# Kernel optimization log

Hardware: AMD Instinct MI355X
Metric: run time of the kernel (lower is better)

## Reference

```python
import jax, jax.numpy as jnp
import numpy as np

N_NODES = 50000
N_EDGES = 800000
IN_FEATS = 256
H_FEATS = 256
NUM_CLASSES = 128


def setup_inputs() -> dict:
    key = jax.random.key(0)
    ks = jax.random.split(key, 5)
    x = jax.random.normal(ks[0], (N_NODES, IN_FEATS), dtype=jnp.float32)
    src = jax.random.randint(ks[1], (N_EDGES,), 0, N_NODES, dtype=jnp.int64)
    dst = jax.random.randint(ks[2], (N_EDGES,), 0, N_NODES, dtype=jnp.int64)
    W1 = jax.random.normal(ks[3], (IN_FEATS, H_FEATS), dtype=jnp.float32) * (1.0 / np.sqrt(IN_FEATS))
    b1 = jnp.zeros((H_FEATS,), dtype=jnp.float32)
    W2 = jax.random.normal(ks[4], (H_FEATS, NUM_CLASSES), dtype=jnp.float32) * (1.0 / np.sqrt(H_FEATS))
    b2 = jnp.zeros((NUM_CLASSES,), dtype=jnp.float32)
    return {"x": x, "src": src, "dst": dst, "W1": W1, "b1": b1, "W2": W2, "b2": b2}


def _graph_conv(x, src, dst, norm_src, norm_dst, W, b):
    # DGL GraphConv, norm='both': D_out^{-1/2} A D_in^{-1/2} X W + b
    # project first (in_feats >= out_feats -> cheaper messages), math identical
    h = (x * norm_src[:, None]) @ W                      # [N, out]
    agg = jax.ops.segment_sum(h[src], dst, num_segments=N_NODES)  # gather + scatter-add
    return agg * norm_dst[:, None] + b


def reference(x, src, dst, W1, b1, W2, b2):
    ones = jnp.ones((N_EDGES,), dtype=x.dtype)
    deg_out = jax.ops.segment_sum(ones, src, num_segments=N_NODES)
    deg_in = jax.ops.segment_sum(ones, dst, num_segments=N_NODES)
    norm_src = jnp.clip(deg_out, 1.0, None) ** -0.5
    norm_dst = jnp.clip(deg_in, 1.0, None) ** -0.5

    h = _graph_conv(x, src, dst, norm_src, norm_dst, W1, b1)
    h = jax.nn.relu(h)
    out = _graph_conv(h, src, dst, norm_src, norm_dst, W2, b2)
    return out
```

## Files before the change

### kernel.cpp

```cpp
#include <hip/hip_runtime.h>

#define NNODES 50000
#define MPAD   50048
#define NEDGES 800000
#define KDIM   256
#define FH     256
#define FOUT   128

#define SHIFT  8
#define NBUCK  196
#define NB1    200
#define EPB    4000
#define CELLS  (NBUCK * NB1)
#define NSCAN  (2 * CELLS)
#define SCANB  ((NSCAN + 511) / 512)

typedef __bf16 bf16x8 __attribute__((ext_vector_type(8)));
typedef float floatx4 __attribute__((ext_vector_type(4)));

__device__ __forceinline__ float bf2f(unsigned short u) {
    union { unsigned int i; float f; } v;
    v.i = ((unsigned int)u) << 16;
    return v.f;
}
__device__ __forceinline__ unsigned short f2bf(float f) {
    union { float f; unsigned int i; } v;
    v.f = f;
    unsigned int r = v.i + 0x7FFFu + ((v.i >> 16) & 1u);
    return (unsigned short)(r >> 16);
}

__global__ __launch_bounds__(256) void l1_count(const int* __restrict__ src,
                                                const int* __restrict__ dst,
                                                int* __restrict__ cell) {
    __shared__ int histD[256], histS[256];
    const int b = blockIdx.x, tid = threadIdx.x;
    const int base = b * EPB;
    histD[tid] = 0; histS[tid] = 0;
    __syncthreads();
    for (int g = tid; g < EPB / 4; g += 256) {
        uint4 s4 = *(const uint4*)(src + base + g * 4);
        uint4 d4 = *(const uint4*)(dst + base + g * 4);
        atomicAdd(&histD[d4.x >> SHIFT], 1);
        atomicAdd(&histD[d4.y >> SHIFT], 1);
        atomicAdd(&histD[d4.z >> SHIFT], 1);
        atomicAdd(&histD[d4.w >> SHIFT], 1);
        atomicAdd(&histS[s4.x >> SHIFT], 1);
        atomicAdd(&histS[s4.y >> SHIFT], 1);
        atomicAdd(&histS[s4.z >> SHIFT], 1);
        atomicAdd(&histS[s4.w >> SHIFT], 1);
    }
    __syncthreads();
    if (tid < NBUCK) {
        cell[tid * NB1 + b] = histD[tid];
        cell[CELLS + tid * NB1 + b] = histS[tid];
    }
}

__global__ __launch_bounds__(512) void scanA(int* __restrict__ data,
                                             int* __restrict__ sums, int n) {
    __shared__ int s[512];
    int tid = threadIdx.x;
    int i = blockIdx.x * 512 + tid;
    int v = (i < n) ? data[i] : 0;
    s[tid] = v;
    __syncthreads();
    for (int off = 1; off < 512; off <<= 1) {
        int t = (tid >= off) ? s[tid - off] : 0;
        __syncthreads();
        s[tid] += t;
        __syncthreads();
    }
    if (i < n) data[i] = s[tid] - v;
    if (tid == 511) sums[blockIdx.x] = s[511];
}

__global__ __launch_bounds__(512) void scanB(int* __restrict__ sums, int nb) {
    __shared__ int s[512];
    int tid = threadIdx.x;
    int v = (tid < nb) ? sums[tid] : 0;
    s[tid] = v;
    __syncthreads();
    for (int off = 1; off < 512; off <<= 1) {
        int t = (tid >= off) ? s[tid - off] : 0;
        __syncthreads();
        s[tid] += t;
        __syncthreads();
    }
    if (tid < nb) sums[tid] = s[tid] - v;
}

__global__ __launch_bounds__(512) void scanC(int* __restrict__ data,
                                             const int* __restrict__ sums, int n) {
    int i = blockIdx.x * 512 + threadIdx.x;
    if (i < n) data[i] += sums[blockIdx.x];
}

__global__ __launch_bounds__(256) void l1_scatter(const int* __restrict__ src,
                                                  const int* __restrict__ dst,
                                                  const int* __restrict__ cell,
                                                  unsigned int* __restrict__ tmp1,
                                                  unsigned char* __restrict__ tmp2) {
    __shared__ int histD[256], histS[256];
    __shared__ int exD[256], exS[256];
    __shared__ unsigned int bufD[EPB];
    __shared__ unsigned short bufS[EPB];
    const int b = blockIdx.x, tid = threadIdx.x;
    const int base = b * EPB;

    histD[tid] = 0; histS[tid] = 0;
    __syncthreads();
    for (int g = tid; g < EPB / 4; g += 256) {
        uint4 s4 = *(const uint4*)(src + base + g * 4);
        uint4 d4 = *(const uint4*)(dst + base + g * 4);
        atomicAdd(&histD[d4.x >> SHIFT], 1);
        atomicAdd(&histD[d4.y >> SHIFT], 1);
        atomicAdd(&histD[d4.z >> SHIFT], 1);
        atomicAdd(&histD[d4.w >> SHIFT], 1);
        atomicAdd(&histS[s4.x >> SHIFT], 1);
        atomicAdd(&histS[s4.y >> SHIFT], 1);
        atomicAdd(&histS[s4.z >> SHIFT], 1);
        atomicAdd(&histS[s4.w >> SHIFT], 1);
    }
    __syncthreads();
    int vD = histD[tid], vS = histS[tid];
    exD[tid] = vD; exS[tid] = vS;
    __syncthreads();
    for (int off = 1; off < 256; off <<= 1) {
        int tD = (tid >= off) ? exD[tid - off] : 0;
        int tS = (tid >= off) ? exS[tid - off] : 0;
        __syncthreads();
        exD[tid] += tD; exS[tid] += tS;
        __syncthreads();
    }
    int eD = exD[tid] - vD, eS = exS[tid] - vS;
    __syncthreads();
    exD[tid] = eD; exS[tid] = eS;
    histD[tid] = eD; histS[tid] = eS;
    __syncthreads();
    for (int g = tid; g < EPB / 4; g += 256) {
        uint4 s4 = *(const uint4*)(src + base + g * 4);
        uint4 d4 = *(const uint4*)(dst + base + g * 4);
        unsigned int ss[4] = {s4.x, s4.y, s4.z, s4.w};
        unsigned int dd[4] = {d4.x, d4.y, d4.z, d4.w};
#pragma unroll
        for (int j = 0; j < 4; ++j) {
            int p = atomicAdd(&histD[dd[j] >> SHIFT], 1);
            bufD[p] = (ss[j] << 16) | dd[j];
            int q = atomicAdd(&histS[ss[j] >> SHIFT], 1);
            bufS[q] = (unsigned short)ss[j];
        }
    }
    __syncthreads();
    for (int e = tid; e < EPB; e += 256) {
        unsigned int p = bufD[e];
        int k = (p & 0xFFFFu) >> SHIFT;
        tmp1[cell[k * NB1 + b] + (e - exD[k])] = p;
    }
    for (int e = tid; e < EPB; e += 256) {
        unsigned int s = bufS[e];
        int k = s >> SHIFT;
        tmp2[(cell[CELLS + k * NB1 + b] - NEDGES) + (e - exS[k])] = (unsigned char)(s & 255u);
    }
}

__global__ __launch_bounds__(256) void l2_dst(const unsigned int* __restrict__ tmp1,
                                              const int* __restrict__ cell,
                                              int* __restrict__ row_ptr,
                                              float* __restrict__ norm_dst,
                                              int* __restrict__ csr_src) {
    __shared__ int cnt[256], ofs[256], cur[256];
    const int k = blockIdx.x, tid = threadIdx.x;
    const int start = cell[k * NB1];
    const int end = (k + 1 < NBUCK) ? cell[(k + 1) * NB1] : NEDGES;
    cnt[tid] = 0;
    __syncthreads();
    for (int e = start + tid; e < end; e += 256)
        atomicAdd(&cnt[tmp1[e] & 255u], 1);
    __syncthreads();
    int v = cnt[tid];
    ofs[tid] = v;
    __syncthreads();
    for (int off = 1; off < 256; off <<= 1) {
        int t = (tid >= off) ? ofs[tid - off] : 0;
        __syncthreads();
        ofs[tid] += t;
        __syncthreads();
    }
    int excl = ofs[tid] - v;
    int node = k * 256 + tid;
    if (node < NNODES) {
        row_ptr[node] = start + excl;
        int d = v < 1 ? 1 : v;
        norm_dst[node] = 1.0f / sqrtf((float)d);
    }
    cur[tid] = start + excl;
    if (k == 0 && tid == 0) row_ptr[NNODES] = NEDGES;
    __syncthreads();
    for (int e = start + tid; e < end; e += 256) {
        unsigned int p = tmp1[e];
        int pos = atomicAdd(&cur[p & 255u], 1);
        csr_src[pos] = (int)(p >> 16);
    }
}

__global__ __launch_bounds__(256) void l2_src(const unsigned char* __restrict__ tmp2,
                                              const int* __restrict__ cell,
                                              float* __restrict__ norm_src) {
    __shared__ int cnt[256];
    const int k = blockIdx.x, tid = threadIdx.x;
    const int start = cell[CELLS + k * NB1] - NEDGES;
    const int end = (k + 1 < NBUCK) ? cell[CELLS + (k + 1) * NB1] - NEDGES : NEDGES;
    cnt[tid] = 0;
    __syncthreads();
    for (int e = start + tid; e < end; e += 256)
        atomicAdd(&cnt[tmp2[e]], 1);
    __syncthreads();
    int node = k * 256 + tid;
    if (node < NNODES) {
        int d = cnt[tid] < 1 ? 1 : cnt[tid];
        norm_src[node] = 1.0f / sqrtf((float)d);
    }
}

__global__ __launch_bounds__(256) void cast_wt_both(const float* __restrict__ W1,
                                                    unsigned short* __restrict__ Wt1,
                                                    const float* __restrict__ W2,
                                                    unsigned short* __restrict__ Wt2) {
    __shared__ float tile[32][33];
    int b = blockIdx.x;
    const float* W; unsigned short* Wt; int N;
    if (b < 64) { W = W1; Wt = Wt1; N = FH; }
    else        { b -= 64; W = W2; Wt = Wt2; N = FOUT; }
    int kt = (b & 7) * 32;
    int nt = (b >> 3) * 32;
    int tx = threadIdx.x & 31;
    int ty = threadIdx.x >> 5;
    for (int r = ty; r < 32; r += 8)
        tile[r][tx] = W[(size_t)(kt + r) * N + nt + tx];
    __syncthreads();
    for (int r = ty; r < 32; r += 8)
        Wt[(size_t)(nt + r) * KDIM + kt + tx] = f2bf(tile[tx][r]);
}

__device__ __forceinline__ uint4 stage_a8(const float* A, int row, int k, float scale, bool valid) {
    if (!valid) return make_uint4(0u, 0u, 0u, 0u);
    const float* p = A + (size_t)row * KDIM + k;
    float4 v0 = *(const float4*)p;
    float4 v1 = *(const float4*)(p + 4);
    union { uint4 u; unsigned short s[8]; } r;
    r.s[0] = f2bf(v0.x * scale); r.s[1] = f2bf(v0.y * scale);
    r.s[2] = f2bf(v0.z * scale); r.s[3] = f2bf(v0.w * scale);
    r.s[4] = f2bf(v1.x * scale); r.s[5] = f2bf(v1.y * scale);
    r.s[6] = f2bf(v1.z * scale); r.s[7] = f2bf(v1.w * scale);
    return r.u;
}
__device__ __forceinline__ uint4 stage_a8(const unsigned short* A, int row, int k, float, bool) {
    return *(const uint4*)(A + (size_t)row * KDIM + k);
}

template <typename TA, bool SCALE>
__global__ __launch_bounds__(256) void gemm_mfma(const TA* __restrict__ A,
                                                 const unsigned short* __restrict__ Bt,
                                                 const float* __restrict__ norm,
                                                 unsigned short* __restrict__ C,
                                                 int N) {
    __shared__ __align__(16) unsigned short As[128][32];
    __shared__ __align__(16) unsigned short Bs[128][32];

    const int tid = threadIdx.x;
    const int lane = tid & 63;
    const int wave = tid >> 6;
    const int wm = wave & 1, wn = wave >> 1;
    const int m0 = blockIdx.x * 128;
    const int n0 = blockIdx.y * 128;

    const int srow = tid >> 2;
    const int sk = (tid & 3) << 3;

    const int r0 = m0 + srow;
    const int r1 = r0 + 64;
    bool va0 = true, va1 = true;
    float sc0 = 0.f, sc1 = 0.f;
    if (SCALE) {
        va0 = (r0 < NNODES); va1 = (r1 < NNODES);
        sc0 = va0 ? norm[r0] : 0.f;
        sc1 = va1 ? norm[r1] : 0.f;
    }

    const unsigned short* Bg = Bt + (size_t)(n0 + srow) * KDIM + sk;

    floatx4 acc[4][4] = {};

    const int ar = wm * 64 + (lane & 15);
    const int br = wn * 64 + (lane & 15);
    const int fk = (lane >> 4) << 3;

    for (int kk = 0; kk < KDIM; kk += 32) {
        uint4 a0 = stage_a8(A, va0 ? r0 : 0, kk + sk, sc0, va0);
        uint4 a1 = stage_a8(A, va1 ? r1 : 0, kk + sk, sc1, va1);
        uint4 b0 = *(const uint4*)(Bg + kk);
        uint4 b1 = *(const uint4*)(Bg + (size_t)64 * KDIM + kk);
        __syncthreads();
        *(uint4*)&As[srow][sk] = a0;
        *(uint4*)&As[srow + 64][sk] = a1;
        *(uint4*)&Bs[srow][sk] = b0;
        *(uint4*)&Bs[srow + 64][sk] = b1;
        __syncthreads();

        bf16x8 af[4], bfr[4];
#pragma unroll
        for (int i = 0; i < 4; ++i) {
            af[i]  = *(const bf16x8*)&As[ar + i * 16][fk];
            bfr[i] = *(const bf16x8*)&Bs[br + i * 16][fk];
        }
#pragma unroll
        for (int i = 0; i < 4; ++i)
#pragma unroll
            for (int j = 0; j < 4; ++j)
                acc[i][j] = __builtin_amdgcn_mfma_f32_16x16x32_bf16(af[i], bfr[j], acc[i][j], 0, 0, 0);
    }

    const int rb = (lane >> 4) << 2;
    const int cc = lane & 15;
#pragma unroll
    for (int i = 0; i < 4; ++i) {
        int mb = m0 + wm * 64 + i * 16 + rb;
#pragma unroll
        for (int j = 0; j < 4; ++j) {
            int col = n0 + wn * 64 + j * 16 + cc;
#pragma unroll
            for (int r = 0; r < 4; ++r) {
                int m = mb + r;
                if (m < NNODES)
                    C[(size_t)m * N + col] = f2bf(acc[i][j][r]);
            }
        }
    }
}

__global__ __launch_bounds__(256) void agg1_kernel(const unsigned short* __restrict__ H,
                                                   const int* __restrict__ row_ptr,
                                                   const int* __restrict__ csr_src,
                                                   const float* __restrict__ norm_dst,
                                                   const float* __restrict__ norm_src,
                                                   const float* __restrict__ bias,
                                                   unsigned short* __restrict__ out) {
    const int F = 256;
    int node = blockIdx.x * 4 + (threadIdx.x >> 6);
    int lane = threadIdx.x & 63;
    int f0 = lane * 4;
    if (node >= NNODES) {
        if (node < MPAD) {
            ushort4 z = {0, 0, 0, 0};
            *(ushort4*)(out + (size_t)node * F + f0) = z;
        }
        return;
    }
    int e0 = row_ptr[node];
    int e1 = row_ptr[node + 1];

    float acc0 = 0.f, acc1 = 0.f, acc2 = 0.f, acc3 = 0.f;
    const unsigned short* Hl = H + f0;

    int e = e0;
    for (; e + 7 < e1; e += 8) {
        ushort4 v[8];
#pragma unroll
        for (int u = 0; u < 8; ++u)
            v[u] = *(const ushort4*)(Hl + (size_t)csr_src[e + u] * F);
#pragma unroll
        for (int u = 0; u < 8; ++u) {
            acc0 += bf2f(v[u].x); acc1 += bf2f(v[u].y);
            acc2 += bf2f(v[u].z); acc3 += bf2f(v[u].w);
        }
    }
    for (; e + 3 < e1; e += 4) {
        ushort4 v[4];
#pragma unroll
        for (int u = 0; u < 4; ++u)
            v[u] = *(const ushort4*)(Hl + (size_t)csr_src[e + u] * F);
#pragma unroll
        for (int u = 0; u < 4; ++u) {
            acc0 += bf2f(v[u].x); acc1 += bf2f(v[u].y);
            acc2 += bf2f(v[u].z); acc3 += bf2f(v[u].w);
        }
    }
    for (; e < e1; ++e) {
        ushort4 v = *(const ushort4*)(Hl + (size_t)csr_src[e] * F);
        acc0 += bf2f(v.x); acc1 += bf2f(v.y); acc2 += bf2f(v.z); acc3 += bf2f(v.w);
    }

    float nd = norm_dst[node];
    float ns = norm_src[node];
    float o0 = fmaxf(fmaf(acc0, nd, bias[f0 + 0]), 0.0f) * ns;
    float o1 = fmaxf(fmaf(acc1, nd, bias[f0 + 1]), 0.0f) * ns;
    float o2 = fmaxf(fmaf(acc2, nd, bias[f0 + 2]), 0.0f) * ns;
    float o3 = fmaxf(fmaf(acc3, nd, bias[f0 + 3]), 0.0f) * ns;
    ushort4 o;
    o.x = f2bf(o0); o.y = f2bf(o1); o.z = f2bf(o2); o.w = f2bf(o3);
    *(ushort4*)(out + (size_t)node * F + f0) = o;
}

__global__ __launch_bounds__(256) void agg2_kernel(const unsigned short* __restrict__ H,
                                                   const int* __restrict__ row_ptr,
                                                   const int* __restrict__ csr_src,
                                                   const float* __restrict__ norm_dst,
                                                   const float* __restrict__ bias,
                                                   float* __restrict__ out) {
    const int F = 128;
    int node = blockIdx.x * 8 + (threadIdx.x >> 5);
    if (node >= NNODES) return;
    int lane = threadIdx.x & 31;
    int f0 = lane * 4;
    int e0 = row_ptr[node];
    int e1 = row_ptr[node + 1];

    float acc0 = 0.f, acc1 = 0.f, acc2 = 0.f, acc3 = 0.f;
    const unsigned short* Hl = H + f0;

    int e = e0;
    for (; e + 7 < e1; e += 8) {
        ushort4 v[8];
#pragma unroll
        for (int u = 0; u < 8; ++u)
            v[u] = *(const ushort4*)(Hl + (size_t)csr_src[e + u] * F);
#pragma unroll
        for (int u = 0; u < 8; ++u) {
            acc0 += bf2f(v[u].x); acc1 += bf2f(v[u].y);
            acc2 += bf2f(v[u].z); acc3 += bf2f(v[u].w);
        }
    }
    for (; e + 3 < e1; e += 4) {
        ushort4 v[4];
#pragma unroll
        for (int u = 0; u < 4; ++u)
            v[u] = *(const ushort4*)(Hl + (size_t)csr_src[e + u] * F);
#pragma unroll
        for (int u = 0; u < 4; ++u) {
            acc0 += bf2f(v[u].x); acc1 += bf2f(v[u].y);
            acc2 += bf2f(v[u].z); acc3 += bf2f(v[u].w);
        }
    }
    for (; e < e1; ++e) {
        ushort4 v = *(const ushort4*)(Hl + (size_t)csr_src[e] * F);
        acc0 += bf2f(v.x); acc1 += bf2f(v.y); acc2 += bf2f(v.z); acc3 += bf2f(v.w);
    }

    float nd = norm_dst[node];
    float4 o;
    o.x = fmaf(acc0, nd, bias[f0 + 0]);
    o.y = fmaf(acc1, nd, bias[f0 + 1]);
    o.z = fmaf(acc2, nd, bias[f0 + 2]);
    o.w = fmaf(acc3, nd, bias[f0 + 3]);
    *(float4*)(out + (size_t)node * F + f0) = o;
}

extern "C" void kernel_launch(void* const* d_in, const int* in_sizes, int n_in,
                              void* d_out, int out_size, void* d_ws, size_t ws_size,
                              hipStream_t stream) {
    const float* x   = (const float*)d_in[0];
    const int*   src = (const int*)d_in[1];
    const int*   dst = (const int*)d_in[2];
    const float* W1  = (const float*)d_in[3];
    const float* b1  = (const float*)d_in[4];
    const float* W2  = (const float*)d_in[5];
    const float* b2  = (const float*)d_in[6];
    float* out = (float*)d_out;

    char* ws = (char*)d_ws;
    size_t off = 0;
    auto alloc = [&](size_t bytes) {
        char* p = ws + off;
        off += (bytes + 255) & ~(size_t)255;
        return p;
    };
    float* norm_src  = (float*)alloc(NNODES * 4);
    float* norm_dst  = (float*)alloc(NNODES * 4);
    int*   cell      = (int*)alloc((size_t)NSCAN * 4);
    int*   ssum      = (int*)alloc(512 * 4);
    unsigned int*  tmp1 = (unsigned int*)alloc((size_t)NEDGES * 4);
    unsigned char* tmp2 = (unsigned char*)alloc((size_t)NEDGES);
    int*   row_ptr   = (int*)alloc((NNODES + 16) * 4);
    int*   csr_src   = (int*)alloc(NEDGES * 4);
    unsigned short* h   = (unsigned short*)alloc((size_t)NNODES * FH * 2);
    unsigned short* h1  = (unsigned short*)alloc((size_t)MPAD * FH * 2);
    unsigned short* Wt1 = (unsigned short*)alloc((size_t)FH * KDIM * 2);
    unsigned short* Wt2 = (unsigned short*)alloc((size_t)FOUT * KDIM * 2);
    unsigned short* h2  = h;

    cast_wt_both<<<96, 256, 0, stream>>>(W1, Wt1, W2, Wt2);

    l1_count<<<NB1, 256, 0, stream>>>(src, dst, cell);
    scanA<<<SCANB, 512, 0, stream>>>(cell, ssum, NSCAN);
    scanB<<<1, 512, 0, stream>>>(ssum, SCANB);
    scanC<<<SCANB, 512, 0, stream>>>(cell, ssum, NSCAN);
    l1_scatter<<<NB1, 256, 0, stream>>>(src, dst, cell, tmp1, tmp2);
    l2_dst<<<NBUCK, 256, 0, stream>>>(tmp1, cell, row_ptr, norm_dst, csr_src);
    l2_src<<<NBUCK, 256, 0, stream>>>(tmp2, cell, norm_src);

    gemm_mfma<float, true><<<dim3(MPAD / 128, FH / 128), 256, 0, stream>>>(x, Wt1, norm_src, h, FH);
    agg1_kernel<<<MPAD / 4, 256, 0, stream>>>(h, row_ptr, csr_src, norm_dst, norm_src, b1, h1);

    gemm_mfma<unsigned short, false><<<dim3(MPAD / 128, FOUT / 128), 256, 0, stream>>>(h1, Wt2, nullptr, h2, FOUT);
    agg2_kernel<<<(NNODES + 7) / 8, 256, 0, stream>>>(h2, row_ptr, csr_src, norm_dst, b2, out);
}
```

Baseline: 266.4 us.

## Store intermediate features in 32-column chunked layout for cache-local gathers

The GEMM outputs and the layer-2 GEMM input now use a chunk-major layout, [chunk][node][32], instead of row-major. The aggregation kernels are relaunched with a second grid dimension over feature chunks, so each pass gathers from a 3.2 MB slice of the feature table rather than the full array. The aim is to keep the random neighbour gathers resident in L2 instead of spilling to HBM. The costs are that the GEMM epilogue stores become strided 2-byte writes, and row_ptr and csr_src are re-read once per chunk.

```diff
diff --git a/kernel.cpp b/kernel.cpp
--- a/kernel.cpp
+++ b/kernel.cpp
@@ -6,6 +6,8 @@
 #define KDIM   256
 #define FH     256
 #define FOUT   128
+
+#define FCH 32
 
 #define SHIFT  8
 #define NBUCK  196
@@ -256,7 +258,7 @@
     return r.u;
 }
 __device__ __forceinline__ uint4 stage_a8(const unsigned short* A, int row, int k, float, bool) {
-    return *(const uint4*)(A + (size_t)row * KDIM + k);
+    return *(const uint4*)(A + ((size_t)(k >> 5) * MPAD + row) * FCH + (k & 31));
 }
 
 template <typename TA, bool SCALE>
@@ -329,11 +331,12 @@
 #pragma unroll
         for (int j = 0; j < 4; ++j) {
             int col = n0 + wn * 64 + j * 16 + cc;
+            size_t cbase = ((size_t)(col >> 5) * MPAD) * FCH + (col & 31);
 #pragma unroll
             for (int r = 0; r < 4; ++r) {
                 int m = mb + r;
                 if (m < NNODES)
-                    C[(size_t)m * N + col] = f2bf(acc[i][j][r]);
+                    C[cbase + (size_t)m * FCH] = f2bf(acc[i][j][r]);
             }
         }
     }
@@ -346,29 +349,28 @@
                                                    const float* __restrict__ norm_src,
                                                    const float* __restrict__ bias,
                                                    unsigned short* __restrict__ out) {
-    const int F = 256;
-    int node = blockIdx.x * 4 + (threadIdx.x >> 6);
-    int lane = threadIdx.x & 63;
-    int f0 = lane * 4;
+    const int c = blockIdx.y;
+    const int node = blockIdx.x * 32 + (threadIdx.x >> 3);
+    const int f = (threadIdx.x & 7) * 4;
+    const unsigned short* Hc = H + (size_t)c * MPAD * FCH + f;
+    unsigned short* outp = out + (size_t)c * MPAD * FCH + (size_t)node * FCH + f;
+
     if (node >= NNODES) {
-        if (node < MPAD) {
-            ushort4 z = {0, 0, 0, 0};
-            *(ushort4*)(out + (size_t)node * F + f0) = z;
-        }
+        ushort4 z = {0, 0, 0, 0};
+        *(ushort4*)outp = z;
         return;
     }
     int e0 = row_ptr[node];
     int e1 = row_ptr[node + 1];
 
     float acc0 = 0.f, acc1 = 0.f, acc2 = 0.f, acc3 = 0.f;
-    const unsigned short* Hl = H + f0;
 
     int e = e0;
     for (; e + 7 < e1; e += 8) {
         ushort4 v[8];
 #pragma unroll
         for (int u = 0; u < 8; ++u)
-            v[u] = *(const ushort4*)(Hl + (size_t)csr_src[e + u] * F);
+            v[u] = *(const ushort4*)(Hc + (size_t)csr_src[e + u] * FCH);
 #pragma unroll
         for (int u = 0; u < 8; ++u) {
             acc0 += bf2f(v[u].x); acc1 += bf2f(v[u].y);
@@ -379,7 +381,7 @@
         ushort4 v[4];
 #pragma unroll
         for (int u = 0; u < 4; ++u)
-            v[u] = *(const ushort4*)(Hl + (size_t)csr_src[e + u] * F);
+            v[u] = *(const ushort4*)(Hc + (size_t)csr_src[e + u] * FCH);
 #pragma unroll
         for (int u = 0; u < 4; ++u) {
             acc0 += bf2f(v[u].x); acc1 += bf2f(v[u].y);
@@ -387,19 +389,20 @@
         }
     }
     for (; e < e1; ++e) {
-        ushort4 v = *(const ushort4*)(Hl + (size_t)csr_src[e] * F);
+        ushort4 v = *(const ushort4*)(Hc + (size_t)csr_src[e] * FCH);
         acc0 += bf2f(v.x); acc1 += bf2f(v.y); acc2 += bf2f(v.z); acc3 += bf2f(v.w);
     }
 
     float nd = norm_dst[node];
     float ns = norm_src[node];
-    float o0 = fmaxf(fmaf(acc0, nd, bias[f0 + 0]), 0.0f) * ns;
-    float o1 = fmaxf(fmaf(acc1, nd, bias[f0 + 1]), 0.0f) * ns;
-    float o2 = fmaxf(fmaf(acc2, nd, bias[f0 + 2]), 0.0f) * ns;
-    float o3 = fmaxf(fmaf(acc3, nd, bias[f0 + 3]), 0.0f) * ns;
+    int fg = c * FCH + f;
+    float o0 = fmaxf(fmaf(acc0, nd, bias[fg + 0]), 0.0f) * ns;
+    float o1 = fmaxf(fmaf(acc1, nd, bias[fg + 1]), 0.0f) * ns;
+    float o2 = fmaxf(fmaf(acc2, nd, bias[fg + 2]), 0.0f) * ns;
+    float o3 = fmaxf(fmaf(acc3, nd, bias[fg + 3]), 0.0f) * ns;
     ushort4 o;
     o.x = f2bf(o0); o.y = f2bf(o1); o.z = f2bf(o2); o.w = f2bf(o3);
-    *(ushort4*)(out + (size_t)node * F + f0) = o;
+    *(ushort4*)outp = o;
 }
 
 __global__ __launch_bounds__(256) void agg2_kernel(const unsigned short* __restrict__ H,
@@ -408,23 +411,23 @@
                                                    const float* __restrict__ norm_dst,
                                                    const float* __restrict__ bias,
                                                    float* __restrict__ out) {
-    const int F = 128;
-    int node = blockIdx.x * 8 + (threadIdx.x >> 5);
+    const int c = blockIdx.y;
+    const int node = blockIdx.x * 32 + (threadIdx.x >> 3);
     if (node >= NNODES) return;
-    int lane = threadIdx.x & 31;
-    int f0 = lane * 4;
+    const int f = (threadIdx.x & 7) * 4;
+    const unsigned short* Hc = H + (size_t)c * MPAD * FCH + f;
+
     int e0 = row_ptr[node];
     int e1 = row_ptr[node + 1];
 
     float acc0 = 0.f, acc1 = 0.f, acc2 = 0.f, acc3 = 0.f;
-    const unsigned short* Hl = H + f0;
 
     int e = e0;
     for (; e + 7 < e1; e += 8) {
         ushort4 v[8];
 #pragma unroll
         for (int u = 0; u < 8; ++u)
-            v[u] = *(const ushort4*)(Hl + (size_t)csr_src[e + u] * F);
+            v[u] = *(const ushort4*)(Hc + (size_t)csr_src[e + u] * FCH);
 #pragma unroll
         for (int u = 0; u < 8; ++u) {
             acc0 += bf2f(v[u].x); acc1 += bf2f(v[u].y);
@@ -435,7 +438,7 @@
         ushort4 v[4];
 #pragma unroll
         for (int u = 0; u < 4; ++u)
-            v[u] = *(const ushort4*)(Hl + (size_t)csr_src[e + u] * F);
+            v[u] = *(const ushort4*)(Hc + (size_t)csr_src[e + u] * FCH);
 #pragma unroll
         for (int u = 0; u < 4; ++u) {
             acc0 += bf2f(v[u].x); acc1 += bf2f(v[u].y);
@@ -443,17 +446,18 @@
         }
     }
     for (; e < e1; ++e) {
-        ushort4 v = *(const ushort4*)(Hl + (size_t)csr_src[e] * F);
+        ushort4 v = *(const ushort4*)(Hc + (size_t)csr_src[e] * FCH);
         acc0 += bf2f(v.x); acc1 += bf2f(v.y); acc2 += bf2f(v.z); acc3 += bf2f(v.w);
     }
 
     float nd = norm_dst[node];
+    int fg = c * FCH + f;
     float4 o;
-    o.x = fmaf(acc0, nd, bias[f0 + 0]);
-    o.y = fmaf(acc1, nd, bias[f0 + 1]);
-    o.z = fmaf(acc2, nd, bias[f0 + 2]);
-    o.w = fmaf(acc3, nd, bias[f0 + 3]);
-    *(float4*)(out + (size_t)node * F + f0) = o;
+    o.x = fmaf(acc0, nd, bias[fg + 0]);
+    o.y = fmaf(acc1, nd, bias[fg + 1]);
+    o.z = fmaf(acc2, nd, bias[fg + 2]);
+    o.w = fmaf(acc3, nd, bias[fg + 3]);
+    *(float4*)(out + (size_t)node * FOUT + fg) = o;
 }
 
 extern "C" void kernel_launch(void* const* d_in, const int* in_sizes, int n_in,
@@ -483,7 +487,7 @@
     unsigned char* tmp2 = (unsigned char*)alloc((size_t)NEDGES);
     int*   row_ptr   = (int*)alloc((NNODES + 16) * 4);
     int*   csr_src   = (int*)alloc(NEDGES * 4);
-    unsigned short* h   = (unsigned short*)alloc((size_t)NNODES * FH * 2);
+    unsigned short* h   = (unsigned short*)alloc((size_t)MPAD * FH * 2);
     unsigned short* h1  = (unsigned short*)alloc((size_t)MPAD * FH * 2);
     unsigned short* Wt1 = (unsigned short*)alloc((size_t)FH * KDIM * 2);
     unsigned short* Wt2 = (unsigned short*)alloc((size_t)FOUT * KDIM * 2);
@@ -500,8 +504,8 @@
     l2_src<<<NBUCK, 256, 0, stream>>>(tmp2, cell, norm_src);
 
     gemm_mfma<float, true><<<dim3(MPAD / 128, FH / 128), 256, 0, stream>>>(x, Wt1, norm_src, h, FH);
-    agg1_kernel<<<MPAD / 4, 256, 0, stream>>>(h, row_ptr, csr_src, norm_dst, norm_src, b1, h1);
+    agg1_kernel<<<dim3(MPAD / 32, FH / FCH), 256, 0, stream>>>(h, row_ptr, csr_src, norm_dst, norm_src, b1, h1);
 
     gemm_mfma<unsigned short, false><<<dim3(MPAD / 128, FOUT / 128), 256, 0, stream>>>(h1, Wt2, nullptr, h2, FOUT);
-    agg2_kernel<<<(NNODES + 7) / 8, 256, 0, stream>>>(h2, row_ptr, csr_src, norm_dst, b2, out);
-}
+    agg2_kernel<<<dim3((NNODES + 31) / 32, FOUT / FCH), 256, 0, stream>>>(h2, row_ptr, csr_src, norm_dst, b2, out);
+}
```

Result: slower. 275.9 us (+3.5%).

## Merge preprocessing kernels and widen layer-1 GEMM tile to cover all columns

Applied to the files above, without the earlier changes.

Folds the weight transpose-cast into the edge-count kernel and the source-degree pass into the destination CSR build, which removes two kernel launches. The first GEMM now computes all 256 output columns per block, so the fp32 x tile is loaded and converted to bf16 once instead of twice. The cost is more accumulator registers and LDS per block and half as many GEMM blocks, which may lower occupancy. The h buffer is enlarged to the padded size.

```diff
diff --git a/kernel.cpp b/kernel.cpp
--- a/kernel.cpp
+++ b/kernel.cpp
@@ -30,11 +30,35 @@
     return (unsigned short)(r >> 16);
 }
 
-__global__ __launch_bounds__(256) void l1_count(const int* __restrict__ src,
-                                                const int* __restrict__ dst,
-                                                int* __restrict__ cell) {
+__global__ __launch_bounds__(256) void l1_count_cast(const int* __restrict__ src,
+                                                     const int* __restrict__ dst,
+                                                     int* __restrict__ cell,
+                                                     const float* __restrict__ W1,
+                                                     unsigned short* __restrict__ Wt1,
+                                                     const float* __restrict__ W2,
+                                                     unsigned short* __restrict__ Wt2) {
     __shared__ int histD[256], histS[256];
-    const int b = blockIdx.x, tid = threadIdx.x;
+    __shared__ float tile[32][33];
+    const int tid = threadIdx.x;
+
+    if (blockIdx.x >= NB1) {
+        int b = blockIdx.x - NB1;
+        const float* W; unsigned short* Wt; int N;
+        if (b < 64) { W = W1; Wt = Wt1; N = FH; }
+        else        { b -= 64; W = W2; Wt = Wt2; N = FOUT; }
+        int kt = (b & 7) * 32;
+        int nt = (b >> 3) * 32;
+        int tx = tid & 31;
+        int ty = tid >> 5;
+        for (int r = ty; r < 32; r += 8)
+            tile[r][tx] = W[(size_t)(kt + r) * N + nt + tx];
+        __syncthreads();
+        for (int r = ty; r < 32; r += 8)
+            Wt[(size_t)(nt + r) * KDIM + kt + tx] = f2bf(tile[tx][r]);
+        return;
+    }
+
+    const int b = blockIdx.x;
     const int base = b * EPB;
     histD[tid] = 0; histS[tid] = 0;
     __syncthreads();
@@ -164,13 +188,34 @@
     }
 }
 
-__global__ __launch_bounds__(256) void l2_dst(const unsigned int* __restrict__ tmp1,
-                                              const int* __restrict__ cell,
-                                              int* __restrict__ row_ptr,
-                                              float* __restrict__ norm_dst,
-                                              int* __restrict__ csr_src) {
+__global__ __launch_bounds__(256) void l2_both(const unsigned int* __restrict__ tmp1,
+                                               const unsigned char* __restrict__ tmp2,
+                                               const int* __restrict__ cell,
+                                               int* __restrict__ row_ptr,
+                                               float* __restrict__ norm_dst,
+                                               float* __restrict__ norm_src,
+                                               int* __restrict__ csr_src) {
     __shared__ int cnt[256], ofs[256], cur[256];
-    const int k = blockIdx.x, tid = threadIdx.x;
+    const int tid = threadIdx.x;
+
+    if (blockIdx.x >= NBUCK) {
+        const int k = blockIdx.x - NBUCK;
+        const int start = cell[CELLS + k * NB1] - NEDGES;
+        const int end = (k + 1 < NBUCK) ? cell[CELLS + (k + 1) * NB1] - NEDGES : NEDGES;
+        cnt[tid] = 0;
+        __syncthreads();
+        for (int e = start + tid; e < end; e += 256)
+            atomicAdd(&cnt[tmp2[e]], 1);
+        __syncthreads();
+        int node = k * 256 + tid;
+        if (node < NNODES) {
+            int d = cnt[tid] < 1 ? 1 : cnt[tid];
+            norm_src[node] = 1.0f / sqrtf((float)d);
+        }
+        return;
+    }
+
+    const int k = blockIdx.x;
     const int start = cell[k * NB1];
     const int end = (k + 1 < NBUCK) ? cell[(k + 1) * NB1] : NEDGES;
     cnt[tid] = 0;
@@ -202,45 +247,6 @@
         int pos = atomicAdd(&cur[p & 255u], 1);
         csr_src[pos] = (int)(p >> 16);
     }
-}
-
-__global__ __launch_bounds__(256) void l2_src(const unsigned char* __restrict__ tmp2,
-                                              const int* __restrict__ cell,
-                                              float* __restrict__ norm_src) {
-    __shared__ int cnt[256];
-    const int k = blockIdx.x, tid = threadIdx.x;
-    const int start = cell[CELLS + k * NB1] - NEDGES;
-    const int end = (k + 1 < NBUCK) ? cell[CELLS + (k + 1) * NB1] - NEDGES : NEDGES;
-    cnt[tid] = 0;
-    __syncthreads();
-    for (int e = start + tid; e < end; e += 256)
-        atomicAdd(&cnt[tmp2[e]], 1);
-    __syncthreads();
-    int node = k * 256 + tid;
-    if (node < NNODES) {
-        int d = cnt[tid] < 1 ? 1 : cnt[tid];
-        norm_src[node] = 1.0f / sqrtf((float)d);
-    }
-}
-
-__global__ __launch_bounds__(256) void cast_wt_both(const float* __restrict__ W1,
-                                                    unsigned short* __restrict__ Wt1,
-                                                    const float* __restrict__ W2,
-                                                    unsigned short* __restrict__ Wt2) {
-    __shared__ float tile[32][33];
-    int b = blockIdx.x;
-    const float* W; unsigned short* Wt; int N;
-    if (b < 64) { W = W1; Wt = Wt1; N = FH; }
-    else        { b -= 64; W = W2; Wt = Wt2; N = FOUT; }
-    int kt = (b & 7) * 32;
-    int nt = (b >> 3) * 32;
-    int tx = threadIdx.x & 31;
-    int ty = threadIdx.x >> 5;
-    for (int r = ty; r < 32; r += 8)
-        tile[r][tx] = W[(size_t)(kt + r) * N + nt + tx];
-    __syncthreads();
-    for (int r = ty; r < 32; r += 8)
-        Wt[(size_t)(nt + r) * KDIM + kt + tx] = f2bf(tile[tx][r]);
 }
 
 __device__ __forceinline__ uint4 stage_a8(const float* A, int row, int k, float scale, bool valid) {
@@ -259,21 +265,21 @@
     return *(const uint4*)(A + (size_t)row * KDIM + k);
 }
 
-template <typename TA, bool SCALE>
+template <typename TA, bool SCALE, int NT>
 __global__ __launch_bounds__(256) void gemm_mfma(const TA* __restrict__ A,
                                                  const unsigned short* __restrict__ Bt,
                                                  const float* __restrict__ norm,
                                                  unsigned short* __restrict__ C,
                                                  int N) {
     __shared__ __align__(16) unsigned short As[128][32];
-    __shared__ __align__(16) unsigned short Bs[128][32];
+    __shared__ __align__(16) unsigned short Bs[128 * NT][32];
 
     const int tid = threadIdx.x;
     const int lane = tid & 63;
     const int wave = tid >> 6;
     const int wm = wave & 1, wn = wave >> 1;
     const int m0 = blockIdx.x * 128;
-    const int n0 = blockIdx.y * 128;
+    const int n0 = blockIdx.y * (128 * NT);
 
     const int srow = tid >> 2;
     const int sk = (tid & 3) << 3;
@@ -290,7 +296,7 @@
 
     const unsigned short* Bg = Bt + (size_t)(n0 + srow) * KDIM + sk;
 
-    floatx4 acc[4][4] = {};
+    floatx4 acc[NT][4][4] = {};
 
     const int ar = wm * 64 + (lane & 15);
     const int br = wn * 64 + (lane & 15);
@@ -299,41 +305,52 @@
     for (int kk = 0; kk < KDIM; kk += 32) {
         uint4 a0 = stage_a8(A, va0 ? r0 : 0, kk + sk, sc0, va0);
         uint4 a1 = stage_a8(A, va1 ? r1 : 0, kk + sk, sc1, va1);
-        uint4 b0 = *(const uint4*)(Bg + kk);
-        uint4 b1 = *(const uint4*)(Bg + (size_t)64 * KDIM + kk);
+        uint4 bld[2 * NT];
+#pragma unroll
+        for (int t = 0; t < 2 * NT; ++t)
+            bld[t] = *(const uint4*)(Bg + (size_t)(64 * t) * KDIM + kk);
         __syncthreads();
         *(uint4*)&As[srow][sk] = a0;
         *(uint4*)&As[srow + 64][sk] = a1;
-        *(uint4*)&Bs[srow][sk] = b0;
-        *(uint4*)&Bs[srow + 64][sk] = b1;
-        __syncthreads();
-
-        bf16x8 af[4], bfr[4];
-#pragma unroll
-        for (int i = 0; i < 4; ++i) {
-            af[i]  = *(const bf16x8*)&As[ar + i * 16][fk];
-            bfr[i] = *(const bf16x8*)&Bs[br + i * 16][fk];
-        }
+#pragma unroll
+        for (int t = 0; t < 2 * NT; ++t)
+            *(uint4*)&Bs[srow + 64 * t][sk] = bld[t];
+        __syncthreads();
+
+        bf16x8 af[4];
 #pragma unroll
         for (int i = 0; i < 4; ++i)
+            af[i] = *(const bf16x8*)&As[ar + i * 16][fk];
+#pragma unroll
+        for (int t = 0; t < NT; ++t) {
+            bf16x8 bfr[4];
 #pragma unroll
             for (int j = 0; j < 4; ++j)
-                acc[i][j] = __builtin_amdgcn_mfma_f32_16x16x32_bf16(af[i], bfr[j], acc[i][j], 0, 0, 0);
+                bfr[j] = *(const bf16x8*)&Bs[t * 128 + br + j * 16][fk];
+#pragma unroll
+            for (int i = 0; i < 4; ++i)
+#pragma unroll
+                for (int j = 0; j < 4; ++j)
+                    acc[t][i][j] = __builtin_amdgcn_mfma_f32_16x16x32_bf16(af[i], bfr[j], acc[t][i][j], 0, 0, 0);
+        }
     }
 
     const int rb = (lane >> 4) << 2;
     const int cc = lane & 15;
 #pragma unroll
-    for (int i = 0; i < 4; ++i) {
-        int mb = m0 + wm * 64 + i * 16 + rb;
-#pragma unroll
-        for (int j = 0; j < 4; ++j) {
-            int col = n0 + wn * 64 + j * 16 + cc;
-#pragma unroll
-            for (int r = 0; r < 4; ++r) {
-                int m = mb + r;
-                if (m < NNODES)
-                    C[(size_t)m * N + col] = f2bf(acc[i][j][r]);
+    for (int t = 0; t < NT; ++t) {
+#pragma unroll
+        for (int i = 0; i < 4; ++i) {
+            int mb = m0 + wm * 64 + i * 16 + rb;
+#pragma unroll
+            for (int j = 0; j < 4; ++j) {
+                int col = n0 + t * 128 + wn * 64 + j * 16 + cc;
+#pragma unroll
+                for (int r = 0; r < 4; ++r) {
+                    int m = mb + r;
+                    if (m < NNODES)
+                        C[(size_t)m * N + col] = f2bf(acc[t][i][j][r]);
+                }
             }
         }
     }
@@ -483,25 +500,22 @@
     unsigned char* tmp2 = (unsigned char*)alloc((size_t)NEDGES);
     int*   row_ptr   = (int*)alloc((NNODES + 16) * 4);
     int*   csr_src   = (int*)alloc(NEDGES * 4);
-    unsigned short* h   = (unsigned short*)alloc((size_t)NNODES * FH * 2);
+    unsigned short* h   = (unsigned short*)alloc((size_t)MPAD * FH * 2);
     unsigned short* h1  = (unsigned short*)alloc((size_t)MPAD * FH * 2);
     unsigned short* Wt1 = (unsigned short*)alloc((size_t)FH * KDIM * 2);
     unsigned short* Wt2 = (unsigned short*)alloc((size_t)FOUT * KDIM * 2);
     unsigned short* h2  = h;
 
-    cast_wt_both<<<96, 256, 0, stream>>>(W1, Wt1, W2, Wt2);
-
-    l1_count<<<NB1, 256, 0, stream>>>(src, dst, cell);
+    l1_count_cast<<<NB1 + 96, 256, 0, stream>>>(src, dst, cell, W1, Wt1, W2, Wt2);
     scanA<<<SCANB, 512, 0, stream>>>(cell, ssum, NSCAN);
     scanB<<<1, 512, 0, stream>>>(ssum, SCANB);
     scanC<<<SCANB, 512, 0, stream>>>(cell, ssum, NSCAN);
     l1_scatter<<<NB1, 256, 0, stream>>>(src, dst, cell, tmp1, tmp2);
-    l2_dst<<<NBUCK, 256, 0, stream>>>(tmp1, cell, row_ptr, norm_dst, csr_src);
-    l2_src<<<NBUCK, 256, 0, stream>>>(tmp2, cell, norm_src);
-
-    gemm_mfma<float, true><<<dim3(MPAD / 128, FH / 128), 256, 0, stream>>>(x, Wt1, norm_src, h, FH);
+    l2_both<<<2 * NBUCK, 256, 0, stream>>>(tmp1, tmp2, cell, row_ptr, norm_dst, norm_src, csr_src);
+
+    gemm_mfma<float, true, 2><<<dim3(MPAD / 128, 1), 256, 0, stream>>>(x, Wt1, norm_src, h, FH);
     agg1_kernel<<<MPAD / 4, 256, 0, stream>>>(h, row_ptr, csr_src, norm_dst, norm_src, b1, h1);
 
-    gemm_mfma<unsigned short, false><<<dim3(MPAD / 128, FOUT / 128), 256, 0, stream>>>(h1, Wt2, nullptr, h2, FOUT);
+    gemm_mfma<unsigned short, false, 1><<<dim3(MPAD / 128, 1), 256, 0, stream>>>(h1, Wt2, nullptr, h2, FOUT);
     agg2_kernel<<<(NNODES + 7) / 8, 256, 0, stream>>>(h2, row_ptr, csr_src, norm_dst, b2, out);
 }
```

Result: slower. 286.7 us (+7.6%).
